# Performance work log

Measured on AMD Instinct MI355X. Metric: run time of the kernel, lower is better.

The kernel has to match this reference:

```python
import jax, jax.numpy as jnp
import numpy as np

# Faithful GCN forward (eval mode, dropout = identity).
# GraphConvolution(x, adj): adj @ (x @ W) + b
# GraphConvolution_edge(edge_feat, adj): edge_feat = cat(x_i, x_j) over all (i,j) pairs,
#   support = edge_feat @ W  (shape [N*N, H]), out[i] = sum_j adj[i,j] * support[i,j] + b.
# materialized: out = (x @ W_top) * rowsum(adj)[:, None] + adj @ (x @ W_bot) + b.

N, NFEAT, NHID = 1536, 512, 64

def _edge_conv(x, adj, W, b):
    H = x.shape[-1]
    A = x @ W[:H]          # [N, H] contribution of x_i
    B = x @ W[H:]          # [N, H] contribution of x_j
    deg = jnp.sum(adj, axis=1, keepdims=True)  # [N, 1]
    return A * deg + adj @ B + b


def setup_inputs() -> dict:
    key = jax.random.key(0)
    ks = jax.random.split(key, 10)
    s1 = 1.0 / np.sqrt(NFEAT)
    s2 = 1.0 / np.sqrt(2 * NHID)
    return {
        "x_init": jax.random.normal(ks[0], (N, NFEAT), jnp.float32),
        "adj": jax.random.uniform(ks[1], (N, N), jnp.float32) / N,
        "adj1": jax.random.uniform(ks[2], (N, N), jnp.float32) / N,
        "fully_connected_graph": jnp.ones((N, N), jnp.float32),
        "W1": jax.random.uniform(ks[3], (NFEAT, NHID), jnp.float32, -s1, s1),
        "b1": jax.random.uniform(ks[4], (NHID,), jnp.float32, -s1, s1),
        "W2": jax.random.uniform(ks[5], (2 * NHID, NHID), jnp.float32, -s2, s2),
        "b2": jax.random.uniform(ks[6], (NHID,), jnp.float32, -s2, s2),
        "W3": jax.random.uniform(ks[7], (2 * NHID, NHID), jnp.float32, -s2, s2),
        "b3": jax.random.uniform(ks[8], (NHID,), jnp.float32, -s2, s2),
    }


def reference(x_init, adj, adj1, fully_connected_graph, W1, b1, W2, b2, W3, b3):
    # gc1: node graph conv + relu (dropout is identity in eval)
    x = jax.nn.relu(adj1 @ (x_init @ W1) + b1)          # [N, NHID]
    # gc_e2: pairwise edge conv + elu
    x = jax.nn.elu(_edge_conv(x, adj1, W2, b2))          # [N, NHID]
    # gc_e3: pairwise edge conv (no activation)
    x = _edge_conv(x, adj1, W3, b3)                      # [N, NHID]
    return jax.nn.log_softmax(x, axis=1)
```

## Files before the change

kernel.cpp:

```cpp
#include <hip/hip_runtime.h>
#include <cmath>

constexpr int NN   = 1536;
constexpr int FF   = 512;
constexpr int HH   = 64;
constexpr int RPB  = 16;
constexpr int NB   = NN / RPB;
constexpr int NT   = 1024;
constexpr int KST  = NN / 32;
constexpr int KST1 = FF / 32;

using f32x4  = __attribute__((ext_vector_type(4))) float;
using bf16x8 = __attribute__((ext_vector_type(8))) short;
using u16x4  = __attribute__((ext_vector_type(4))) unsigned short;
typedef unsigned short u16;

__device__ __forceinline__ u16 f2bf(float f) {
  unsigned u = __builtin_bit_cast(unsigned, f);
  return (u16)((u + 0x7fffu + ((u >> 16) & 1u)) >> 16);
}

__device__ __forceinline__ size_t bidx(int k, int c) {
  return (size_t)((c >> 5) * (KST * 2) + (k >> 5) * 2 + ((c >> 4) & 1)) * 512 +
         ((k & 31) >> 3) * 128 + (c & 15) * 8 + (k & 7);
}

__device__ __forceinline__ void gl_lds16(const void* g, void* l) {
  __builtin_amdgcn_global_load_lds(
      (const __attribute__((address_space(1))) unsigned*)g,
      (__attribute__((address_space(3))) unsigned*)l, 16, 0, 0);
}

__device__ __forceinline__ void pack_wnb(u16* WnB, const float* Wsrc, int tid) {
  int jp = tid & 127, kb = (tid >> 7) * 8;
  int srow0 = (jp >> 6) * 64, col = jp & 63;
#pragma unroll
  for (int i = 0; i < 8; ++i) {
    int k = kb + i;
    WnB[((k >> 5) * 8 + (jp >> 4)) * 512 + ((k & 31) >> 3) * 128 +
        (jp & 15) * 8 + (k & 7)] = f2bf(Wsrc[(size_t)(srow0 + k) * HH + col]);
  }
}

__global__ __launch_bounds__(NT, 4) void k_pre(
    const float* __restrict__ x, const float* __restrict__ adj,
    const float* __restrict__ W1,
    u16* __restrict__ adjT, u16* __restrict__ t1T, float* __restrict__ deg) {
  __shared__ u16 Al[KST1 * 512];
  __shared__ u16 Bl[KST1 * 4 * 512];
  __shared__ u16 Jl[KST * 512];
  __shared__ float red0[4][4][16][16];
  const int tid = threadIdx.x, lane = tid & 63, wave = tid >> 6;
  const int i0 = blockIdx.x * RPB;

  {
    int j0 = lane * 8;
    const float* src = x + (size_t)(i0 + wave) * FF + j0;
    bf16x8 v;
#pragma unroll
    for (int jj = 0; jj < 8; ++jj) v[jj] = (short)f2bf(src[jj]);
    *(bf16x8*)&Al[(j0 >> 5) * 512 + ((j0 & 31) >> 3) * 128 + wave * 8] = v;
  }
  {
    int k = tid >> 1, c0 = (tid & 1) * 32;
    const float* src = W1 + (size_t)k * HH + c0;
    int base = (k >> 5) * 2048 + ((k & 31) >> 3) * 128 + (k & 7);
#pragma unroll 8
    for (int cc = 0; cc < 32; ++cc) {
      int c = c0 + cc;
      Bl[base + (c >> 4) * 512 + (c & 15) * 8] = f2bf(src[cc]);
    }
  }
  {
    int j0 = lane * 24;
    const float* src = adj + (size_t)(i0 + wave) * NN + j0;
    float ds = 0.f;
#pragma unroll
    for (int g = 0; g < 3; ++g) {
      bf16x8 v;
#pragma unroll
      for (int jj = 0; jj < 8; ++jj) {
        float f = src[g * 8 + jj];
        ds += f;
        v[jj] = (short)f2bf(f);
      }
      int k = j0 + g * 8;
      *(bf16x8*)&Jl[(k >> 5) * 512 + ((k & 31) >> 3) * 128 + wave * 8] = v;
    }
#pragma unroll
    for (int off = 32; off; off >>= 1) ds += __shfl_xor(ds, off, 64);
    if (lane == 0) deg[i0 + wave] = ds;
  }
  __syncthreads();

  {
    const float4* srcv = (const float4*)Jl;
    float4* dstv = (float4*)(adjT + (size_t)blockIdx.x * KST * 512);
#pragma unroll
    for (int s = 0; s < 3; ++s) dstv[tid + s * NT] = srcv[tid + s * NT];
  }
  {
    int ks = wave >> 2, cg = wave & 3;
    f32x4 acc = {0.f, 0.f, 0.f, 0.f};
#pragma unroll
    for (int s = 0; s < 4; ++s) {
      int t = ks * 4 + s;
      bf16x8 a = *(const bf16x8*)&Al[t * 512 + lane * 8];
      bf16x8 b = *(const bf16x8*)&Bl[(t * 4 + cg) * 512 + lane * 8];
      acc = __builtin_amdgcn_mfma_f32_16x16x32_bf16(a, b, acc, 0, 0, 0);
    }
#pragma unroll
    for (int q = 0; q < 4; ++q)
      red0[ks][cg][(lane >> 4) * 4 + q][lane & 15] = acc[q];
  }
  __syncthreads();
  {
    int r = wave, c = lane;
    float v = red0[0][c >> 4][r][c & 15] + red0[1][c >> 4][r][c & 15] +
              red0[2][c >> 4][r][c & 15] + red0[3][c >> 4][r][c & 15];
    t1T[bidx(i0 + r, c)] = f2bf(v);
  }
}

template <int MODE>
__global__ __launch_bounds__(NT, 4) void k_layer(
    const u16* __restrict__ adjT, const u16* __restrict__ TT,
    const float* __restrict__ Ain, const float* __restrict__ deg,
    const float* __restrict__ bias, const float* __restrict__ Wn,
    float* __restrict__ outA, u16* __restrict__ outBT,
    float* __restrict__ out) {
  __shared__ __attribute__((aligned(16))) char LB[155712];
  float* red8 = (float*)(LB + 98304);
  u16*   WnB  = (u16*)(LB + 133120);
  u16*   xA   = (u16*)(LB + 149504);
  float* xloc = (float*)(LB + 151552);

  const int tid = threadIdx.x, lane = tid & 63, wave = tid >> 6;
  const int i0 = blockIdx.x * RPB;

  const u16* ja = adjT + (size_t)blockIdx.x * (KST * 512);
  bf16x8 afr[3];
#pragma unroll
  for (int s = 0; s < 3; ++s)
    afr[s] = *(const bf16x8*)(ja + (wave * 3 + s) * 512 + lane * 8);

  if (MODE < 2) pack_wnb(WnB, Wn, tid);
  float dg = 0.f;
  if (MODE >= 1) dg = deg[i0 + wave];

  f32x4 acc[4] = {{0, 0, 0, 0}, {0, 0, 0, 0}, {0, 0, 0, 0}, {0, 0, 0, 0}};
#pragma unroll
  for (int h = 0; h < 2; ++h) {
    {
      const char* gsrc = (const char*)TT + (size_t)h * 98304 + wave * 6144 +
                         (size_t)lane * 16;
      char* ldst = LB + wave * 6144;
      asm volatile("s_waitcnt lgkmcnt(0)" ::: "memory");
#pragma unroll
      for (int r = 0; r < 6; ++r) gl_lds16(gsrc + r * 1024, ldst + r * 1024);
    }
    asm volatile("s_waitcnt vmcnt(0)" ::: "memory");
    __builtin_amdgcn_sched_barrier(0);
#pragma unroll
    for (int s = 0; s < 3; ++s)
#pragma unroll
      for (int chi = 0; chi < 2; ++chi) {
        bf16x8 b = *(const bf16x8*)(LB + wave * 6144 + (s * 2 + chi) * 1024 +
                                    lane * 16);
        acc[h * 2 + chi] = __builtin_amdgcn_mfma_f32_16x16x32_bf16(
            afr[s], b, acc[h * 2 + chi], 0, 0, 0);
      }
  }

  if (wave < 8) {
#pragma unroll
    for (int cg = 0; cg < 4; ++cg)
#pragma unroll
      for (int q = 0; q < 4; ++q)
        red8[((wave * 4 + cg) * 16 + ((lane >> 4) * 4 + q)) * 17 +
             (lane & 15)] = acc[cg][q];
  }
  __syncthreads();
  if (wave >= 8) {
#pragma unroll
    for (int cg = 0; cg < 4; ++cg)
#pragma unroll
      for (int q = 0; q < 4; ++q)
        red8[(((wave - 8) * 4 + cg) * 16 + ((lane >> 4) * 4 + q)) * 17 +
             (lane & 15)] += acc[cg][q];
  }
  __syncthreads();

  {
    float v = bias[lane];
#pragma unroll
    for (int s = 0; s < 8; ++s)
      v += red8[((s * 4 + (lane >> 4)) * 16 + wave) * 17 + (lane & 15)];
    if (MODE >= 1) v += Ain[(size_t)(i0 + wave) * HH + lane] * dg;
    if (MODE == 0) v = fmaxf(v, 0.f);
    if (MODE == 1) v = v > 0.f ? v : expm1f(v);
    xloc[wave * 65 + lane] = v;
    if (MODE < 2)
      xA[(lane >> 5) * 512 + ((lane & 31) >> 3) * 128 + wave * 8 +
         (lane & 7)] = f2bf(v);
  }
  __syncthreads();

  if (MODE < 2) {
    if (wave < 8) {
      f32x4 a2 = {0.f, 0.f, 0.f, 0.f};
#pragma unroll
      for (int s = 0; s < 2; ++s) {
        bf16x8 a = *(const bf16x8*)&xA[s * 512 + lane * 8];
        bf16x8 b = *(const bf16x8*)&WnB[(s * 8 + wave) * 512 + lane * 8];
        a2 = __builtin_amdgcn_mfma_f32_16x16x32_bf16(a, b, a2, 0, 0, 0);
      }
      int row = (lane >> 4) * 4, colg = lane & 15;
      if (wave < 4) {
        int c = wave * 16 + colg;
#pragma unroll
        for (int q = 0; q < 4; ++q)
          outA[(size_t)(i0 + row + q) * HH + c] = a2[q];
      } else {
        int c = (wave - 4) * 16 + colg;
        u16x4 v;
#pragma unroll
        for (int q = 0; q < 4; ++q) v[q] = f2bf(a2[q]);
        *(u16x4*)&outBT[bidx(i0 + row, c)] = v;
      }
    }
  } else {
    float v = xloc[wave * 65 + lane];
    float m = v;
#pragma unroll
    for (int off = 32; off; off >>= 1) m = fmaxf(m, __shfl_xor(m, off, 64));
    float e = expf(v - m);
    float ssum = e;
#pragma unroll
    for (int off = 32; off; off >>= 1) ssum += __shfl_xor(ssum, off, 64);
    out[(size_t)(i0 + wave) * HH + lane] = v - m - logf(ssum);
  }
}

extern "C" void kernel_launch(void* const* d_in, const int* in_sizes, int n_in,
                              void* d_out, int out_size, void* d_ws,
                              size_t ws_size, hipStream_t stream) {
  const float* x   = (const float*)d_in[0];
  const float* adj = (const float*)d_in[2];
  const float* W1  = (const float*)d_in[4];
  const float* b1  = (const float*)d_in[5];
  const float* W2  = (const float*)d_in[6];
  const float* b2  = (const float*)d_in[7];
  const float* W3  = (const float*)d_in[8];
  const float* b3  = (const float*)d_in[9];
  float* out = (float*)d_out;

  char* ws = (char*)d_ws;
  u16* adjT = (u16*)ws;
  u16* t1T  = (u16*)(ws + 4718592);
  u16* B2T  = (u16*)(ws + 4915200);
  u16* B3T  = (u16*)(ws + 5111808);
  float* A2 = (float*)(ws + 5308416);
  float* A3 = (float*)(ws + 5701632);
  float* dg = (float*)(ws + 6094848);

  k_pre<<<NB, NT, 0, stream>>>(x, adj, W1, adjT, t1T, dg);
  k_layer<0><<<NB, NT, 0, stream>>>(adjT, t1T, nullptr, nullptr, b1, W2, A2,
                                    B2T, nullptr);
  k_layer<1><<<NB, NT, 0, stream>>>(adjT, B2T, A2, dg, b2, W3, A3, B3T,
                                    nullptr);
  k_layer<2><<<NB, NT, 0, stream>>>(adjT, B3T, A3, dg, b3, nullptr, nullptr,
                                    nullptr, out);
}
```

Baseline: 30.28 us.

## Process two row tiles per layer block and double-buffer B-operand loads

Result: slower. 36.66 us (+21.1%).

```diff
diff --git a/kernel.cpp b/kernel.cpp
--- a/kernel.cpp
+++ b/kernel.cpp
@@ -5,10 +5,18 @@
 constexpr int FF   = 512;
 constexpr int HH   = 64;
 constexpr int RPB  = 16;
-constexpr int NB   = NN / RPB;
+constexpr int NBP  = NN / RPB;
+constexpr int LRPB = 32;
+constexpr int NBL  = NN / LRPB;
 constexpr int NT   = 1024;
 constexpr int KST  = NN / 32;
 constexpr int KST1 = FF / 32;
+
+constexpr int O_RED  = 98304;
+constexpr int O_WNB  = 133120;
+constexpr int O_XA   = 149504;
+constexpr int O_XLOC = 153600;
+constexpr int LDS_L  = 161920;
 
 using f32x4  = __attribute__((ext_vector_type(4))) float;
 using bf16x8 = __attribute__((ext_vector_type(8))) short;
@@ -129,116 +137,138 @@
     const float* __restrict__ bias, const float* __restrict__ Wn,
     float* __restrict__ outA, u16* __restrict__ outBT,
     float* __restrict__ out) {
-  __shared__ __attribute__((aligned(16))) char LB[155712];
-  float* red8 = (float*)(LB + 98304);
-  u16*   WnB  = (u16*)(LB + 133120);
-  u16*   xA   = (u16*)(LB + 149504);
-  float* xloc = (float*)(LB + 151552);
+  __shared__ __attribute__((aligned(16))) char LB[LDS_L];
+  float* red  = (float*)(LB + O_RED);
+  u16*   WnB  = (u16*)(LB + O_WNB);
+  u16*   xA   = (u16*)(LB + O_XA);
+  float* xloc = (float*)(LB + O_XLOC);
 
   const int tid = threadIdx.x, lane = tid & 63, wave = tid >> 6;
-  const int i0 = blockIdx.x * RPB;
-
-  const u16* ja = adjT + (size_t)blockIdx.x * (KST * 512);
-  bf16x8 afr[3];
+  const int i0 = blockIdx.x * LRPB;
+
+  bf16x8 afr[3][2];
+#pragma unroll
+  for (int rt = 0; rt < 2; ++rt) {
+    const u16* ja = adjT + (size_t)(2 * blockIdx.x + rt) * (KST * 512);
+#pragma unroll
+    for (int s = 0; s < 3; ++s)
+      afr[s][rt] = *(const bf16x8*)(ja + (wave * 3 + s) * 512 + lane * 8);
+  }
+  if (MODE < 2) pack_wnb(WnB, Wn, tid);
+
+  char* const regA = LB + wave * 6144;
+  char* const regB = regA + 3072;
+  const int kb = wave * 3;
+  const char* tb = (const char*)TT + (size_t)lane * 16;
+
+  f32x4 acc[4][2] = {};
 #pragma unroll
   for (int s = 0; s < 3; ++s)
-    afr[s] = *(const bf16x8*)(ja + (wave * 3 + s) * 512 + lane * 8);
-
-  if (MODE < 2) pack_wnb(WnB, Wn, tid);
-  float dg = 0.f;
-  if (MODE >= 1) dg = deg[i0 + wave];
-
-  f32x4 acc[4] = {{0, 0, 0, 0}, {0, 0, 0, 0}, {0, 0, 0, 0}, {0, 0, 0, 0}};
-#pragma unroll
-  for (int h = 0; h < 2; ++h) {
+    gl_lds16(tb + (size_t)((kb + s) * 2 + 0) * 1024, regA + s * 1024);
+#pragma unroll
+  for (int s = 0; s < 3; ++s)
+    gl_lds16(tb + (size_t)((kb + s) * 2 + 1) * 1024, regB + s * 1024);
+
+#pragma unroll
+  for (int cg = 0; cg < 4; ++cg) {
+    if (cg < 3) asm volatile("s_waitcnt vmcnt(3)" ::: "memory");
+    else        asm volatile("s_waitcnt vmcnt(0)" ::: "memory");
+    __builtin_amdgcn_sched_barrier(0);
+    char* reg = (cg & 1) ? regB : regA;
+    bf16x8 b0 = *(const bf16x8*)(reg);
+    bf16x8 b1 = *(const bf16x8*)(reg + 1024);
+    bf16x8 b2 = *(const bf16x8*)(reg + 2048);
+    asm volatile("s_waitcnt lgkmcnt(0)" ::: "memory");
+    __builtin_amdgcn_sched_barrier(0);
+    if (cg < 2) {
+      int q = cg + 2;
+#pragma unroll
+      for (int s = 0; s < 3; ++s)
+        gl_lds16(tb + (size_t)((q >> 1) * 96 + (kb + s) * 2 + (q & 1)) * 1024,
+                 reg + s * 1024);
+    }
+#pragma unroll
+    for (int rt = 0; rt < 2; ++rt) {
+      acc[cg][rt] = __builtin_amdgcn_mfma_f32_16x16x32_bf16(afr[0][rt], b0, acc[cg][rt], 0, 0, 0);
+      acc[cg][rt] = __builtin_amdgcn_mfma_f32_16x16x32_bf16(afr[1][rt], b1, acc[cg][rt], 0, 0, 0);
+      acc[cg][rt] = __builtin_amdgcn_mfma_f32_16x16x32_bf16(afr[2][rt], b2, acc[cg][rt], 0, 0, 0);
+    }
+  }
+
+#pragma unroll
+  for (int rt = 0; rt < 2; ++rt) {
+    if (rt == 1) __syncthreads();
+    if (wave < 8) {
+#pragma unroll
+      for (int cg = 0; cg < 4; ++cg)
+#pragma unroll
+        for (int q = 0; q < 4; ++q)
+          red[((wave * 4 + cg) * 16 + ((lane >> 4) * 4 + q)) * 17 +
+              (lane & 15)] = acc[cg][rt][q];
+    }
+    __syncthreads();
+    if (wave >= 8) {
+#pragma unroll
+      for (int cg = 0; cg < 4; ++cg)
+#pragma unroll
+        for (int q = 0; q < 4; ++q)
+          red[(((wave - 8) * 4 + cg) * 16 + ((lane >> 4) * 4 + q)) * 17 +
+              (lane & 15)] += acc[cg][rt][q];
+    }
+    __syncthreads();
     {
-      const char* gsrc = (const char*)TT + (size_t)h * 98304 + wave * 6144 +
-                         (size_t)lane * 16;
-      char* ldst = LB + wave * 6144;
-      asm volatile("s_waitcnt lgkmcnt(0)" ::: "memory");
-#pragma unroll
-      for (int r = 0; r < 6; ++r) gl_lds16(gsrc + r * 1024, ldst + r * 1024);
-    }
-    asm volatile("s_waitcnt vmcnt(0)" ::: "memory");
-    __builtin_amdgcn_sched_barrier(0);
-#pragma unroll
-    for (int s = 0; s < 3; ++s)
-#pragma unroll
-      for (int chi = 0; chi < 2; ++chi) {
-        bf16x8 b = *(const bf16x8*)(LB + wave * 6144 + (s * 2 + chi) * 1024 +
-                                    lane * 16);
-        acc[h * 2 + chi] = __builtin_amdgcn_mfma_f32_16x16x32_bf16(
-            afr[s], b, acc[h * 2 + chi], 0, 0, 0);
-      }
-  }
-
-  if (wave < 8) {
-#pragma unroll
-    for (int cg = 0; cg < 4; ++cg)
+      int r = rt * 16 + wave;
+      float v = bias[lane];
+#pragma unroll
+      for (int s = 0; s < 8; ++s)
+        v += red[((s * 4 + (lane >> 4)) * 16 + wave) * 17 + (lane & 15)];
+      if (MODE >= 1) v += Ain[(size_t)(i0 + r) * HH + lane] * deg[i0 + r];
+      if (MODE == 0) v = fmaxf(v, 0.f);
+      if (MODE == 1) v = v > 0.f ? v : expm1f(v);
+      xloc[r * 65 + lane] = v;
+      if (MODE < 2)
+        xA[(rt * 2 + (lane >> 5)) * 512 + ((lane & 31) >> 3) * 128 + wave * 8 +
+           (lane & 7)] = f2bf(v);
+    }
+  }
+  __syncthreads();
+
+  if (MODE < 2) {
+    int rt = wave >> 3, cgg = wave & 7;
+    f32x4 a2 = {};
+#pragma unroll
+    for (int s = 0; s < 2; ++s) {
+      bf16x8 a = *(const bf16x8*)&xA[(rt * 2 + s) * 512 + lane * 8];
+      bf16x8 b = *(const bf16x8*)&WnB[(s * 8 + cgg) * 512 + lane * 8];
+      a2 = __builtin_amdgcn_mfma_f32_16x16x32_bf16(a, b, a2, 0, 0, 0);
+    }
+    int row0 = (lane >> 4) * 4, colg = lane & 15;
+    if (cgg < 4) {
+      int c = cgg * 16 + colg;
 #pragma unroll
       for (int q = 0; q < 4; ++q)
-        red8[((wave * 4 + cg) * 16 + ((lane >> 4) * 4 + q)) * 17 +
-             (lane & 15)] = acc[cg][q];
-  }
-  __syncthreads();
-  if (wave >= 8) {
-#pragma unroll
-    for (int cg = 0; cg < 4; ++cg)
-#pragma unroll
-      for (int q = 0; q < 4; ++q)
-        red8[(((wave - 8) * 4 + cg) * 16 + ((lane >> 4) * 4 + q)) * 17 +
-             (lane & 15)] += acc[cg][q];
-  }
-  __syncthreads();
-
-  {
-    float v = bias[lane];
-#pragma unroll
-    for (int s = 0; s < 8; ++s)
-      v += red8[((s * 4 + (lane >> 4)) * 16 + wave) * 17 + (lane & 15)];
-    if (MODE >= 1) v += Ain[(size_t)(i0 + wave) * HH + lane] * dg;
-    if (MODE == 0) v = fmaxf(v, 0.f);
-    if (MODE == 1) v = v > 0.f ? v : expm1f(v);
-    xloc[wave * 65 + lane] = v;
-    if (MODE < 2)
-      xA[(lane >> 5) * 512 + ((lane & 31) >> 3) * 128 + wave * 8 +
-         (lane & 7)] = f2bf(v);
-  }
-  __syncthreads();
-
-  if (MODE < 2) {
-    if (wave < 8) {
-      f32x4 a2 = {0.f, 0.f, 0.f, 0.f};
-#pragma unroll
-      for (int s = 0; s < 2; ++s) {
-        bf16x8 a = *(const bf16x8*)&xA[s * 512 + lane * 8];
-        bf16x8 b = *(const bf16x8*)&WnB[(s * 8 + wave) * 512 + lane * 8];
-        a2 = __builtin_amdgcn_mfma_f32_16x16x32_bf16(a, b, a2, 0, 0, 0);
-      }
-      int row = (lane >> 4) * 4, colg = lane & 15;
-      if (wave < 4) {
-        int c = wave * 16 + colg;
-#pragma unroll
-        for (int q = 0; q < 4; ++q)
-          outA[(size_t)(i0 + row + q) * HH + c] = a2[q];
-      } else {
-        int c = (wave - 4) * 16 + colg;
-        u16x4 v;
-#pragma unroll
-        for (int q = 0; q < 4; ++q) v[q] = f2bf(a2[q]);
-        *(u16x4*)&outBT[bidx(i0 + row, c)] = v;
-      }
+        outA[(size_t)(i0 + rt * 16 + row0 + q) * HH + c] = a2[q];
+    } else {
+      int c = (cgg - 4) * 16 + colg;
+      u16x4 v;
+#pragma unroll
+      for (int q = 0; q < 4; ++q) v[q] = f2bf(a2[q]);
+      *(u16x4*)&outBT[bidx(i0 + rt * 16 + row0, c)] = v;
     }
   } else {
-    float v = xloc[wave * 65 + lane];
-    float m = v;
-#pragma unroll
-    for (int off = 32; off; off >>= 1) m = fmaxf(m, __shfl_xor(m, off, 64));
-    float e = expf(v - m);
-    float ssum = e;
-#pragma unroll
-    for (int off = 32; off; off >>= 1) ssum += __shfl_xor(ssum, off, 64);
-    out[(size_t)(i0 + wave) * HH + lane] = v - m - logf(ssum);
+#pragma unroll
+    for (int rr = 0; rr < 2; ++rr) {
+      int r = wave + rr * 16;
+      float v = xloc[r * 65 + lane];
+      float m = v;
+#pragma unroll
+      for (int off = 32; off; off >>= 1) m = fmaxf(m, __shfl_xor(m, off, 64));
+      float e = expf(v - m);
+      float ssum = e;
+#pragma unroll
+      for (int off = 32; off; off >>= 1) ssum += __shfl_xor(ssum, off, 64);
+      out[(size_t)(i0 + r) * HH + lane] = v - m - logf(ssum);
+    }
   }
 }
 
@@ -264,11 +294,11 @@
   float* A3 = (float*)(ws + 5701632);
   float* dg = (float*)(ws + 6094848);
 
-  k_pre<<<NB, NT, 0, stream>>>(x, adj, W1, adjT, t1T, dg);
-  k_layer<0><<<NB, NT, 0, stream>>>(adjT, t1T, nullptr, nullptr, b1, W2, A2,
-                                    B2T, nullptr);
-  k_layer<1><<<NB, NT, 0, stream>>>(adjT, B2T, A2, dg, b2, W3, A3, B3T,
-                                    nullptr);
-  k_layer<2><<<NB, NT, 0, stream>>>(adjT, B3T, A3, dg, b3, nullptr, nullptr,
-                                    nullptr, out);
-}
+  k_pre<<<NBP, NT, 0, stream>>>(x, adj, W1, adjT, t1T, dg);
+  k_layer<0><<<NBL, NT, 0, stream>>>(adjT, t1T, nullptr, nullptr, b1, W2, A2,
+                                     B2T, nullptr);
+  k_layer<1><<<NBL, NT, 0, stream>>>(adjT, B2T, A2, dg, b2, W3, A3, B3T,
+                                     nullptr);
+  k_layer<2><<<NBL, NT, 0, stream>>>(adjT, B3T, A3, dg, b3, nullptr, nullptr,
+                                     nullptr, out);
+}
```

## Double-buffer per-column-group B tile loads and vectorize float4 input reads

Applied to the files above, without the earlier changes.

After: 30.09 us. No clear change (-0.6%).

```diff
diff --git a/kernel.cpp b/kernel.cpp
--- a/kernel.cpp
+++ b/kernel.cpp
@@ -55,35 +55,46 @@
 
   {
     int j0 = lane * 8;
-    const float* src = x + (size_t)(i0 + wave) * FF + j0;
+    const float4* src = (const float4*)(x + (size_t)(i0 + wave) * FF + j0);
+    float4 f0 = src[0], f1 = src[1];
     bf16x8 v;
-#pragma unroll
-    for (int jj = 0; jj < 8; ++jj) v[jj] = (short)f2bf(src[jj]);
+    v[0] = (short)f2bf(f0.x); v[1] = (short)f2bf(f0.y);
+    v[2] = (short)f2bf(f0.z); v[3] = (short)f2bf(f0.w);
+    v[4] = (short)f2bf(f1.x); v[5] = (short)f2bf(f1.y);
+    v[6] = (short)f2bf(f1.z); v[7] = (short)f2bf(f1.w);
     *(bf16x8*)&Al[(j0 >> 5) * 512 + ((j0 & 31) >> 3) * 128 + wave * 8] = v;
   }
   {
     int k = tid >> 1, c0 = (tid & 1) * 32;
-    const float* src = W1 + (size_t)k * HH + c0;
+    const float4* src = (const float4*)(W1 + (size_t)k * HH + c0);
     int base = (k >> 5) * 2048 + ((k & 31) >> 3) * 128 + (k & 7);
-#pragma unroll 8
-    for (int cc = 0; cc < 32; ++cc) {
-      int c = c0 + cc;
-      Bl[base + (c >> 4) * 512 + (c & 15) * 8] = f2bf(src[cc]);
+#pragma unroll
+    for (int g = 0; g < 8; ++g) {
+      float4 f = src[g];
+      int c = c0 + g * 4;
+      int off = base + (c >> 4) * 512 + (c & 15) * 8;
+      Bl[off]      = f2bf(f.x);
+      Bl[off + 8]  = f2bf(f.y);
+      Bl[off + 16] = f2bf(f.z);
+      Bl[off + 24] = f2bf(f.w);
     }
   }
   {
     int j0 = lane * 24;
-    const float* src = adj + (size_t)(i0 + wave) * NN + j0;
+    const float4* src = (const float4*)(adj + (size_t)(i0 + wave) * NN + j0);
+    float4 f[6];
+#pragma unroll
+    for (int g = 0; g < 6; ++g) f[g] = src[g];
     float ds = 0.f;
+#pragma unroll
+    for (int g = 0; g < 6; ++g) ds += f[g].x + f[g].y + f[g].z + f[g].w;
 #pragma unroll
     for (int g = 0; g < 3; ++g) {
       bf16x8 v;
-#pragma unroll
-      for (int jj = 0; jj < 8; ++jj) {
-        float f = src[g * 8 + jj];
-        ds += f;
-        v[jj] = (short)f2bf(f);
-      }
+      v[0] = (short)f2bf(f[g * 2].x);     v[1] = (short)f2bf(f[g * 2].y);
+      v[2] = (short)f2bf(f[g * 2].z);     v[3] = (short)f2bf(f[g * 2].w);
+      v[4] = (short)f2bf(f[g * 2 + 1].x); v[5] = (short)f2bf(f[g * 2 + 1].y);
+      v[6] = (short)f2bf(f[g * 2 + 1].z); v[7] = (short)f2bf(f[g * 2 + 1].w);
       int k = j0 + g * 8;
       *(bf16x8*)&Jl[(k >> 5) * 512 + ((k & 31) >> 3) * 128 + wave * 8] = v;
     }
@@ -148,28 +159,40 @@
   float dg = 0.f;
   if (MODE >= 1) dg = deg[i0 + wave];
 
-  f32x4 acc[4] = {{0, 0, 0, 0}, {0, 0, 0, 0}, {0, 0, 0, 0}, {0, 0, 0, 0}};
-#pragma unroll
-  for (int h = 0; h < 2; ++h) {
-    {
-      const char* gsrc = (const char*)TT + (size_t)h * 98304 + wave * 6144 +
-                         (size_t)lane * 16;
-      char* ldst = LB + wave * 6144;
-      asm volatile("s_waitcnt lgkmcnt(0)" ::: "memory");
-#pragma unroll
-      for (int r = 0; r < 6; ++r) gl_lds16(gsrc + r * 1024, ldst + r * 1024);
-    }
-    asm volatile("s_waitcnt vmcnt(0)" ::: "memory");
+  char* const regA = LB + wave * 6144;
+  char* const regB = regA + 3072;
+  const int kb = wave * 3;
+  const char* tb = (const char*)TT + (size_t)lane * 16;
+
+  f32x4 acc[4] = {};
+#pragma unroll
+  for (int s = 0; s < 3; ++s)
+    gl_lds16(tb + (size_t)((kb + s) * 2 + 0) * 1024, regA + s * 1024);
+#pragma unroll
+  for (int s = 0; s < 3; ++s)
+    gl_lds16(tb + (size_t)((kb + s) * 2 + 1) * 1024, regB + s * 1024);
+
+#pragma unroll
+  for (int cg = 0; cg < 4; ++cg) {
+    if (cg < 3) asm volatile("s_waitcnt vmcnt(3)" ::: "memory");
+    else        asm volatile("s_waitcnt vmcnt(0)" ::: "memory");
     __builtin_amdgcn_sched_barrier(0);
-#pragma unroll
-    for (int s = 0; s < 3; ++s)
-#pragma unroll
-      for (int chi = 0; chi < 2; ++chi) {
-        bf16x8 b = *(const bf16x8*)(LB + wave * 6144 + (s * 2 + chi) * 1024 +
-                                    lane * 16);
-        acc[h * 2 + chi] = __builtin_amdgcn_mfma_f32_16x16x32_bf16(
-            afr[s], b, acc[h * 2 + chi], 0, 0, 0);
-      }
+    char* reg = (cg & 1) ? regB : regA;
+    bf16x8 b0 = *(const bf16x8*)(reg);
+    bf16x8 b1 = *(const bf16x8*)(reg + 1024);
+    bf16x8 b2 = *(const bf16x8*)(reg + 2048);
+    asm volatile("s_waitcnt lgkmcnt(0)" ::: "memory");
+    __builtin_amdgcn_sched_barrier(0);
+    if (cg < 2) {
+      int q = cg + 2;
+#pragma unroll
+      for (int s = 0; s < 3; ++s)
+        gl_lds16(tb + (size_t)((q >> 1) * 96 + (kb + s) * 2 + (q & 1)) * 1024,
+                 reg + s * 1024);
+    }
+    acc[cg] = __builtin_amdgcn_mfma_f32_16x16x32_bf16(afr[0], b0, acc[cg], 0, 0, 0);
+    acc[cg] = __builtin_amdgcn_mfma_f32_16x16x32_bf16(afr[1], b1, acc[cg], 0, 0, 0);
+    acc[cg] = __builtin_amdgcn_mfma_f32_16x16x32_bf16(afr[2], b2, acc[cg], 0, 0, 0);
   }
 
   if (wave < 8) {
@@ -208,7 +231,7 @@
 
   if (MODE < 2) {
     if (wave < 8) {
-      f32x4 a2 = {0.f, 0.f, 0.f, 0.f};
+      f32x4 a2 = {};
 #pragma unroll
       for (int s = 0; s < 2; ++s) {
         bf16x8 a = *(const bf16x8*)&xA[s * 512 + lane * 8];
```
